# Performance work log

Hardware: AMD Instinct MI355X
Metric: run time of the kernel (lower is better)

## Reference

```python
import jax, jax.numpy as jnp
import numpy as np


def _step(state):
    # state: [B, H, W] in {0.0, 1.0}
    p = jnp.pad(state, ((0, 0), (1, 1), (1, 1)))
    neighbors = (p[:, :-2, :-2] + p[:, :-2, 1:-1] + p[:, :-2, 2:]
                 + p[:, 1:-1, :-2] + p[:, 1:-1, 2:]
                 + p[:, 2:, :-2] + p[:, 2:, 1:-1] + p[:, 2:, 2:])
    alive = state > 0.5
    survives = alive & ((neighbors == 2.0) | (neighbors == 3.0))
    born = (~alive) & (neighbors == 3.0)
    return jnp.where(survives | born, jnp.ones_like(state), jnp.zeros_like(state))


def setup_inputs() -> dict:
    key = jax.random.key(0)
    k1, k2 = jax.random.split(key)
    B, H, W = 32, 1024, 1024
    # Binary occupancy grids in {0.0, 1.0} as the rule expects
    initial_state = (jax.random.uniform(k1, (B, H, W)) > 0.5).astype(jnp.float32)
    target = (jax.random.uniform(k2, (B, H, W)) > 0.5).astype(jnp.float32)
    return {"initial_state": initial_state, "target": target, "generations": 8}


def reference(initial_state, target, generations):
    state = initial_state
    for _ in range(generations):  # small fixed unroll, strict sequential dependency
        state = _step(state)
    error = state - target
    loss = jnp.mean(error * error)
    live_cells = state.sum()
    max_abs_error = jnp.abs(error).max()
    return loss, state, target, live_cells, max_abs_error
```

## Files before the change

kernel.cpp:

```cpp
#include <hip/hip_runtime.h>
#include <cstdint>

typedef unsigned long long u64;

#define BATCH   32
#define H       1024
#define W       1024
#define WPR     16
#define TR      64
#define HALO    8
#define BR      (TR + 2*HALO)
#define BRP     (BR + 2)
#define WP      (WPR + 2)
#define THREADS 512
#define NWAVES  (THREADS/64)
#define GENS    8
#define NTOT    33554432ULL

__global__ __launch_bounds__(THREADS)
void gol_fused(const float* __restrict__ in_state,
               const float* __restrict__ target,
               float* __restrict__ out,
               unsigned int* __restrict__ counters)
{
    __shared__ u64 buf[2][BRP][WP];

    const int tile = blockIdx.x;
    const int tpb  = H / TR;
    const int b    = tile / tpb;
    const int r0   = (tile - b * tpb) * TR;

    const int tid  = threadIdx.x;
    const int wave = tid >> 6;
    const int lane = tid & 63;

    for (int i = tid; i < 2 * BRP * WP; i += THREADS)
        ((u64*)buf)[i] = 0ULL;
    __syncthreads();

    const size_t boff = (size_t)b * H * W;
    const float* inb  = in_state + boff;

    for (int br = wave; br < BR; br += NWAVES) {
        int gr = r0 - HALO + br;
        if (gr < 0 || gr >= H) continue;
        const float* rowp = inb + (size_t)gr * W;
        #pragma unroll
        for (int g = 0; g < 4; ++g) {
            int base = g * 256;
            float f0 = rowp[base       + lane];
            float f1 = rowp[base +  64 + lane];
            float f2 = rowp[base + 128 + lane];
            float f3 = rowp[base + 192 + lane];
            u64 w0 = __ballot(f0 > 0.5f);
            u64 w1 = __ballot(f1 > 0.5f);
            u64 w2 = __ballot(f2 > 0.5f);
            u64 w3 = __ballot(f3 > 0.5f);
            if (lane == 0) {
                buf[0][br + 1][g*4 + 1] = w0;
                buf[0][br + 1][g*4 + 2] = w1;
                buf[0][br + 1][g*4 + 3] = w2;
                buf[0][br + 1][g*4 + 4] = w3;
            }
        }
    }
    __syncthreads();

    int cur = 0;
    for (int step = 0; step < GENS; ++step) {
        for (int idx = tid; idx < BR * WPR; idx += THREADS) {
            int br = idx >> 4;
            int c  = (idx & 15) + 1;
            int r  = br + 1;
            int gr = r0 - HALO + br;

            u64 uL = buf[cur][r-1][c-1], uC = buf[cur][r-1][c], uR = buf[cur][r-1][c+1];
            u64 mL = buf[cur][r  ][c-1], mC = buf[cur][r  ][c], mR = buf[cur][r  ][c+1];
            u64 dL = buf[cur][r+1][c-1], dC = buf[cur][r+1][c], dR = buf[cur][r+1][c+1];

            u64 uw = (uC << 1) | (uL >> 63), ue = (uC >> 1) | (uR << 63);
            u64 mw = (mC << 1) | (mL >> 63), me = (mC >> 1) | (mR << 63);
            u64 dw = (dC << 1) | (dL >> 63), de = (dC >> 1) | (dR << 63);
            u64 o0 = uw ^ uC ^ ue, t0 = (uw & uC) | (ue & (uw ^ uC));
            u64 o1 = mw ^ mC ^ me, t1 = (mw & mC) | (me & (mw ^ mC));
            u64 o2 = dw ^ dC ^ de, t2 = (dw & dC) | (de & (dw ^ dC));

            u64 oa = o0 ^ o1 ^ o2;
            u64 oc = (o0 & o1) | (o2 & (o0 ^ o1));
            u64 ts = t0 ^ t1 ^ t2;
            u64 tc = (t0 & t1) | (t2 & (t0 ^ t1));
            u64 b1 = oc ^ ts;
            u64 cc = oc & ts;
            u64 b2 = cc ^ tc;
            u64 b3 = cc & tc;
            u64 eq3 = oa & b1 & ~(b2 | b3);
            u64 eq4 = (~oa) & (~b1) & b2 & (~b3);
            u64 nxtw = eq3 | (mC & eq4);

            buf[cur ^ 1][r][c] = (gr >= 0 && gr < H) ? nxtw : 0ULL;
        }
        __syncthreads();
        cur ^= 1;
    }

    float* o_state = out + 1;
    float* o_tgt   = out + 1 + NTOT;
    const float* tgtb = target + boff;

    unsigned int mism = 0, live = 0;
    for (int lr = wave; lr < TR; lr += NWAVES) {
        int br = HALO + lr;
        int gr = r0 + lr;
        size_t rowoff = boff + (size_t)gr * W;
        const float* trow = tgtb + (size_t)gr * W;
        #pragma unroll
        for (int g = 0; g < 4; ++g) {
            int base = g * 256;
            #pragma unroll
            for (int s = 0; s < 4; ++s) {
                u64 w = buf[cur][br + 1][g*4 + s + 1];
                int col = base + s * 64 + lane;
                float t = trow[col];
                int sbit = (int)((w >> lane) & 1ULL);
                int tbit = (t > 0.5f) ? 1 : 0;
                o_state[rowoff + col] = (float)sbit;
                o_tgt[rowoff + col]   = t;
                u64 mmw = __ballot(sbit != tbit);
                mism += (unsigned)__popcll(mmw);
                live += (unsigned)__popcll(w);
            }
        }
    }
    if (lane == 0) {
        atomicAdd(&counters[0], mism);
        atomicAdd(&counters[1], live);
    }
}

__global__ void gol_finalize(const unsigned int* __restrict__ counters,
                             float* __restrict__ out)
{
    unsigned int mism = counters[0];
    unsigned int live = counters[1];
    out[0]            = (float)((double)mism / (double)NTOT);
    out[1 + 2*NTOT]   = (float)live;
    out[2 + 2*NTOT]   = (mism > 0) ? 1.0f : 0.0f;
}

extern "C" void kernel_launch(void* const* d_in, const int* in_sizes, int n_in,
                              void* d_out, int out_size, void* d_ws, size_t ws_size,
                              hipStream_t stream) {
    (void)in_sizes; (void)n_in; (void)out_size; (void)ws_size;
    const float* in_state = (const float*)d_in[0];
    const float* target   = (const float*)d_in[1];
    float* out = (float*)d_out;
    unsigned int* counters = (unsigned int*)d_ws;

    hipMemsetAsync(d_ws, 0, 2 * sizeof(unsigned int), stream);

    dim3 grid(BATCH * (H / TR));
    gol_fused<<<grid, THREADS, 0, stream>>>(in_state, target, out, counters);
    gol_finalize<<<1, 1, 0, stream>>>(counters, out);
}
```

Measured before the change: 517.6 us.

## Vectorize global I/O with float4, shrink tiles, fuse finalize into last block

Loads the input and target rows as float4 and packs bits with cross-lane shuffles instead of per-element ballots. Stores both outputs as float4. Halves the tile height and thread count and unrolls the generation loop. Folds the two counters into one wave-level shuffle reduction and replaces the separate finalize kernel with a last-block-done pattern. Smaller tiles raise the halo recompute overhead, and the extra atomic counter adds a little serialization.

```diff
diff --git a/kernel.cpp b/kernel.cpp
--- a/kernel.cpp
+++ b/kernel.cpp
@@ -7,15 +7,20 @@
 #define H       1024
 #define W       1024
 #define WPR     16
-#define TR      64
+#define TR      32
 #define HALO    8
 #define BR      (TR + 2*HALO)
 #define BRP     (BR + 2)
 #define WP      (WPR + 2)
-#define THREADS 512
+#define THREADS 256
 #define NWAVES  (THREADS/64)
 #define GENS    8
+#define GRID    (BATCH * (H / TR))
 #define NTOT    33554432ULL
+
+__device__ __forceinline__ u64 shflxor64(u64 v, int m) {
+    return (u64)__shfl_xor((long long)v, m, 64);
+}
 
 __global__ __launch_bounds__(THREADS)
 void gol_fused(const float* __restrict__ in_state,
@@ -24,6 +29,7 @@
                unsigned int* __restrict__ counters)
 {
     __shared__ u64 buf[2][BRP][WP];
+    __shared__ int isLast;
 
     const int tile = blockIdx.x;
     const int tpb  = H / TR;
@@ -41,34 +47,33 @@
     const size_t boff = (size_t)b * H * W;
     const float* inb  = in_state + boff;
 
+    const int sub   = lane & 15;
+    const int wsub  = lane >> 4;
     for (int br = wave; br < BR; br += NWAVES) {
         int gr = r0 - HALO + br;
         if (gr < 0 || gr >= H) continue;
-        const float* rowp = inb + (size_t)gr * W;
+        const float4* rowp4 = (const float4*)(inb + (size_t)gr * W);
         #pragma unroll
         for (int g = 0; g < 4; ++g) {
-            int base = g * 256;
-            float f0 = rowp[base       + lane];
-            float f1 = rowp[base +  64 + lane];
-            float f2 = rowp[base + 128 + lane];
-            float f3 = rowp[base + 192 + lane];
-            u64 w0 = __ballot(f0 > 0.5f);
-            u64 w1 = __ballot(f1 > 0.5f);
-            u64 w2 = __ballot(f2 > 0.5f);
-            u64 w3 = __ballot(f3 > 0.5f);
-            if (lane == 0) {
-                buf[0][br + 1][g*4 + 1] = w0;
-                buf[0][br + 1][g*4 + 2] = w1;
-                buf[0][br + 1][g*4 + 3] = w2;
-                buf[0][br + 1][g*4 + 4] = w3;
-            }
+            float4 f = rowp4[g * 64 + lane];
+            u64 nib = (u64)((f.x > 0.5f) | ((f.y > 0.5f) << 1) |
+                            ((f.z > 0.5f) << 2) | ((f.w > 0.5f) << 3));
+            u64 v = nib << (sub * 4);
+            v |= shflxor64(v, 1);
+            v |= shflxor64(v, 2);
+            v |= shflxor64(v, 4);
+            v |= shflxor64(v, 8);
+            if (sub == 0)
+                buf[0][br + 1][g * 4 + wsub + 1] = v;
         }
     }
     __syncthreads();
 
     int cur = 0;
     for (int step = 0; step < GENS; ++step) {
-        for (int idx = tid; idx < BR * WPR; idx += THREADS) {
+        #pragma unroll
+        for (int k = 0; k < (BR * WPR) / THREADS; ++k) {
+            int idx = tid + k * THREADS;
             int br = idx >> 4;
             int c  = (idx & 15) + 1;
             int r  = br + 1;
@@ -105,46 +110,57 @@
 
     float* o_state = out + 1;
     float* o_tgt   = out + 1 + NTOT;
-    const float* tgtb = target + boff;
 
+    const int sh = (lane * 4) & 63;
     unsigned int mism = 0, live = 0;
     for (int lr = wave; lr < TR; lr += NWAVES) {
         int br = HALO + lr;
         int gr = r0 + lr;
         size_t rowoff = boff + (size_t)gr * W;
-        const float* trow = tgtb + (size_t)gr * W;
+        const float4* trow4 = (const float4*)(target + rowoff);
+        float4* os4 = (float4*)(o_state + rowoff);
+        float4* ot4 = (float4*)(o_tgt + rowoff);
         #pragma unroll
         for (int g = 0; g < 4; ++g) {
-            int base = g * 256;
-            #pragma unroll
-            for (int s = 0; s < 4; ++s) {
-                u64 w = buf[cur][br + 1][g*4 + s + 1];
-                int col = base + s * 64 + lane;
-                float t = trow[col];
-                int sbit = (int)((w >> lane) & 1ULL);
-                int tbit = (t > 0.5f) ? 1 : 0;
-                o_state[rowoff + col] = (float)sbit;
-                o_tgt[rowoff + col]   = t;
-                u64 mmw = __ballot(sbit != tbit);
-                mism += (unsigned)__popcll(mmw);
-                live += (unsigned)__popcll(w);
-            }
+            u64 w = buf[cur][br + 1][g * 4 + wsub + 1];
+            unsigned bits = (unsigned)((w >> sh) & 0xFULL);
+            float4 t = trow4[g * 64 + lane];
+            unsigned tb = (unsigned)((t.x > 0.5f) | ((t.y > 0.5f) << 1) |
+                                     ((t.z > 0.5f) << 2) | ((t.w > 0.5f) << 3));
+            mism += (unsigned)__popc(bits ^ tb);
+            live += (unsigned)__popc(bits);
+            float4 sv;
+            sv.x = (float)(bits & 1u);
+            sv.y = (float)((bits >> 1) & 1u);
+            sv.z = (float)((bits >> 2) & 1u);
+            sv.w = (float)((bits >> 3) & 1u);
+            os4[g * 64 + lane] = sv;
+            ot4[g * 64 + lane] = t;
         }
     }
+
+    unsigned int comb = (mism << 16) | live;
+    #pragma unroll
+    for (int m = 1; m < 64; m <<= 1)
+        comb += (unsigned int)__shfl_xor((int)comb, m, 64);
     if (lane == 0) {
-        atomicAdd(&counters[0], mism);
-        atomicAdd(&counters[1], live);
+        atomicAdd(&counters[0], comb >> 16);
+        atomicAdd(&counters[1], comb & 0xFFFFu);
     }
-}
 
-__global__ void gol_finalize(const unsigned int* __restrict__ counters,
-                             float* __restrict__ out)
-{
-    unsigned int mism = counters[0];
-    unsigned int live = counters[1];
-    out[0]            = (float)((double)mism / (double)NTOT);
-    out[1 + 2*NTOT]   = (float)live;
-    out[2 + 2*NTOT]   = (mism > 0) ? 1.0f : 0.0f;
+    if (tid == 0) {
+        __threadfence();
+        unsigned prev = atomicAdd(&counters[2], 1u);
+        isLast = (prev == GRID - 1) ? 1 : 0;
+    }
+    __syncthreads();
+    if (isLast && tid == 0) {
+        unsigned int mm = atomicAdd(&counters[0], 0u);
+        unsigned int lv = atomicAdd(&counters[1], 0u);
+        out[0]            = (float)((double)mm / (double)NTOT);
+        out[1 + 2*NTOT]   = (float)lv;
+        out[2 + 2*NTOT]   = (mm > 0) ? 1.0f : 0.0f;
+    }
 }
 
 extern "C" void kernel_launch(void* const* d_in, const int* in_sizes, int n_in,
@@ -156,9 +172,7 @@
     float* out = (float*)d_out;
     unsigned int* counters = (unsigned int*)d_ws;
 
-    hipMemsetAsync(d_ws, 0, 2 * sizeof(unsigned int), stream);
+    hipMemsetAsync(d_ws, 0, 3 * sizeof(unsigned int), stream);
 
-    dim3 grid(BATCH * (H / TR));
-    gol_fused<<<grid, THREADS, 0, stream>>>(in_state, target, out, counters);
-    gol_finalize<<<1, 1, 0, stream>>>(counters, out);
+    gol_fused<<<dim3(GRID), dim3(THREADS), 0, stream>>>(in_state, target, out, counters);
 }
```

Result: slower. 546.8 us (+5.6%).
